# Performance work log

Measured on AMD Instinct MI355X. Metric: run time of the kernel, lower is better.

Reference implementation:

```python
import jax, jax.numpy as jnp
import numpy as np

N = 8192      # total nodes = B * NPG
D = 512       # in_dim = hidden_dim = out_dim
E = 131072    # edges
B = 16        # graphs (selected_idx batch)
NPG = 512     # nodes per graph
S = 128       # selected nodes per graph
L = 3         # conv layers
EPS = 1e-5


def setup_inputs() -> dict:
    key = jax.random.key(0)
    ks = jax.random.split(key, 16)
    scale = 0.02
    return {
        "x": jax.random.normal(ks[0], (N, D), dtype=jnp.float32),
        "edge_index": jax.random.randint(ks[1], (2, E), 0, N),
        "selected_idx": jax.random.randint(ks[2], (B, S), 0, NPG),
        "edge_label": jax.random.randint(ks[3], (E,), 0, 4),
        # per-layer EdgeConv MLP params (stacked over L layers)
        "conv_W1": jax.random.normal(ks[4], (L, 2 * D, D), dtype=jnp.float32) * scale,
        "conv_b1": jnp.full((L, D), 0.01, dtype=jnp.float32),
        "conv_W2": jax.random.normal(ks[5], (L, D, D), dtype=jnp.float32) * scale,
        "conv_b2": jnp.full((L, D), 0.01, dtype=jnp.float32),
        # shared layer norms
        "ln1_g": jnp.ones((D,), dtype=jnp.float32),
        "ln1_b": jnp.zeros((D,), dtype=jnp.float32),
        "ln2_g": jnp.ones((D,), dtype=jnp.float32),
        "ln2_b": jnp.zeros((D,), dtype=jnp.float32),
        # final FFN
        "ffn_W1": jax.random.normal(ks[6], (D, D), dtype=jnp.float32) * scale,
        "ffn_b1": jnp.full((D,), 0.01, dtype=jnp.float32),
        "ffn_W2": jax.random.normal(ks[7], (D, D), dtype=jnp.float32) * scale,
        "ffn_b2": jnp.full((D,), 0.01, dtype=jnp.float32),
    }


def _layer_norm(x, g, b):
    mu = jnp.mean(x, axis=-1, keepdims=True)
    var = jnp.mean(jnp.square(x - mu), axis=-1, keepdims=True)
    return (x - mu) * jax.lax.rsqrt(var + EPS) * g + b


def reference(x, edge_index, selected_idx, edge_label,
              conv_W1, conv_b1, conv_W2, conv_b2,
              ln1_g, ln1_b, ln2_g, ln2_b,
              ffn_W1, ffn_b1, ffn_W2, ffn_b2):
    src = edge_index[0]  # x_j source nodes
    dst = edge_index[1]  # x_i target nodes (aggregation index)
    for l in range(L):
        residual = x
        h = _layer_norm(x, ln1_g, ln1_b)
        hi = h[dst]                                   # [E, D]
        hj = h[src]                                   # [E, D]
        ef = jnp.concatenate([hi, hj - hi], axis=1)   # [E, 2D]
        m = jnp.maximum(ef @ conv_W1[l] + conv_b1[l], 0.0) @ conv_W2[l] + conv_b2[l]
        agg = jax.ops.segment_max(m, dst, num_segments=N)  # max-aggregate [N, D]
        agg = jnp.where(jnp.isfinite(agg), agg, 0.0)       # nodes w/o in-edges -> 0
        x = jnp.maximum(agg, 0.0) + residual
    residual = x
    h = _layer_norm(x, ln2_g, ln2_b)
    y = jnp.maximum(h @ ffn_W1 + ffn_b1, 0.0) @ ffn_W2 + ffn_b2
    x = y + residual
    x = x.reshape(B, NPG, D)
    idx = jnp.broadcast_to(selected_idx[:, :, None], (B, S, D))
    return jnp.take_along_axis(x, idx, axis=1)  # [B, S, D]
```

## Files before the change

### kernel.cpp

```cpp
#include <hip/hip_runtime.h>
#include <stdint.h>

#define NN 8192
#define DD 512
#define EE 131072
#define BBATCH 16
#define NPG 512
#define SSEL 128
#define LL 3

typedef unsigned short u16;
typedef __bf16 bf16x8 __attribute__((ext_vector_type(8)));
typedef float f32x4 __attribute__((ext_vector_type(4)));
typedef float f32x2 __attribute__((ext_vector_type(2)));
typedef u16 u16x8 __attribute__((ext_vector_type(8)));

__device__ __forceinline__ float bf2f(u16 u) {
    union { unsigned i; float f; } v; v.i = ((unsigned)u) << 16; return v.f;
}
__device__ __forceinline__ u16 f2bf(float f) {
    union { unsigned i; float f; } v; v.f = f;
    unsigned i = v.i;
    return (u16)((i + 0x7FFFu + ((i >> 16) & 1u)) >> 16);
}

__device__ __forceinline__ unsigned pk_bf16(float s0, float s1) {
#if __has_builtin(__builtin_amdgcn_cvt_pk_bf16_f32)
    typedef __bf16 bf16x2 __attribute__((ext_vector_type(2)));
    union { bf16x2 v; unsigned u; } r;
    r.v = __builtin_amdgcn_cvt_pk_bf16_f32(s0, s1);
    return r.u;
#else
    unsigned r0 = __float_as_uint(s0);
    r0 = (r0 + 0x7FFFu + ((r0 >> 16) & 1u)) >> 16;
    unsigned r1 = __float_as_uint(s1);
    r1 = (r1 + 0x7FFFu + ((r1 >> 16) & 1u)) & 0xffff0000u;
    return r0 | r1;
#endif
}

__device__ __forceinline__ void async_cp16(const u16* g, u16* l) {
    __builtin_amdgcn_global_load_lds(
        (const __attribute__((address_space(1))) unsigned int*)g,
        (__attribute__((address_space(3))) unsigned int*)l, 16, 0, 0);
}

__global__ __launch_bounds__(256) void ln_fused(const float* __restrict__ xin,
                                                float* __restrict__ agg_io,
                                                float* __restrict__ xout,
                                                const float* __restrict__ g,
                                                const float* __restrict__ b,
                                                u16* __restrict__ h, int doAdd) {
    int row = blockIdx.x * 4 + (threadIdx.x >> 6);
    int lane = threadIdx.x & 63;
    const f32x4* x4 = (const f32x4*)(xin + (size_t)row * DD);
    f32x4 p = x4[lane * 2], q = x4[lane * 2 + 1];
    if (doAdd) {
        const f32x4* a4 = (const f32x4*)(agg_io + (size_t)row * DD);
        f32x4 pa = a4[lane * 2], qa = a4[lane * 2 + 1];
        #pragma unroll
        for (int i = 0; i < 4; ++i) { p[i] += pa[i]; q[i] += qa[i]; }
    }
    if (agg_io) {
        f32x4 z;
        #pragma unroll
        for (int i = 0; i < 4; ++i) z[i] = 0.f;
        f32x4* a4 = (f32x4*)(agg_io + (size_t)row * DD);
        a4[lane * 2] = z;
        a4[lane * 2 + 1] = z;
    }
    f32x4* xo = (f32x4*)(xout + (size_t)row * DD);
    xo[lane * 2] = p;
    xo[lane * 2 + 1] = q;
    float v[8];
    v[0] = p[0]; v[1] = p[1]; v[2] = p[2]; v[3] = p[3];
    v[4] = q[0]; v[5] = q[1]; v[6] = q[2]; v[7] = q[3];
    float s = 0.f, sq = 0.f;
    #pragma unroll
    for (int i = 0; i < 8; ++i) { s += v[i]; sq += v[i] * v[i]; }
    #pragma unroll
    for (int o = 32; o >= 1; o >>= 1) { s += __shfl_xor(s, o); sq += __shfl_xor(sq, o); }
    float mu = s * (1.f / DD);
    float var = sq * (1.f / DD) - mu * mu;
    float rs = rsqrtf(var + 1e-5f);
    int kb = lane * 8;
    u16x8 o8;
    #pragma unroll
    for (int i = 0; i < 8; ++i) o8[i] = f2bf((v[i] - mu) * rs * g[kb + i] + b[kb + i]);
    *(u16x8*)(h + (size_t)row * DD + kb) = o8;
}

__global__ void hist_kernel(const int* __restrict__ dst, int* __restrict__ cnt) {
    int e = blockIdx.x * 256 + threadIdx.x;
    if (e < EE) atomicAdd(&cnt[dst[e]], 1);
}

__global__ __launch_bounds__(1024) void scan_kernel(const int* __restrict__ cnt,
                                                    int* __restrict__ off,
                                                    int* __restrict__ cur) {
    __shared__ int part[1024];
    int t = threadIdx.x;
    int base = t * 8;
    int loc[8]; int s = 0;
    #pragma unroll
    for (int i = 0; i < 8; ++i) { loc[i] = s; s += cnt[base + i]; }
    part[t] = s;
    __syncthreads();
    for (int o = 1; o < 1024; o <<= 1) {
        int v = part[t];
        int u = (t >= o) ? part[t - o] : 0;
        __syncthreads();
        part[t] = v + u;
        __syncthreads();
    }
    int bx = (t > 0) ? part[t - 1] : 0;
    #pragma unroll
    for (int i = 0; i < 8; ++i) { off[base + i] = bx + loc[i]; cur[base + i] = bx + loc[i]; }
    if (t == 0) off[NN] = part[1023];
}

__global__ void scatter_kernel(const int* __restrict__ src, const int* __restrict__ dst,
                               int* __restrict__ cur, int* __restrict__ ssrc,
                               int* __restrict__ sdst) {
    int e = blockIdx.x * 256 + threadIdx.x;
    if (e < EE) {
        int d = dst[e];
        int p = atomicAdd(&cur[d], 1);
        ssrc[p] = src[e];
        sdst[p] = d;
    }
}

struct CvtJobs {
    const float* s[5];
    u16* d[5];
};
__global__ __launch_bounds__(256) void cvt_t5_kernel(CvtJobs jobs) {
    __shared__ u16 tile[32][33];
    const float* src = jobs.s[blockIdx.z];
    u16* dstp = jobs.d[blockIdx.z];
    int bk = blockIdx.x * 32, bn = blockIdx.y * 32;
    int tx = threadIdx.x & 31, ty = threadIdx.x >> 5;
    #pragma unroll
    for (int r = 0; r < 32; r += 8)
        tile[ty + r][tx] = f2bf(src[(size_t)(bk + ty + r) * 512 + bn + tx]);
    __syncthreads();
    #pragma unroll
    for (int r = 0; r < 32; r += 8)
        dstp[(size_t)(bn + ty + r) * 512 + bk + tx] = tile[tx][ty + r];
}

__global__ __launch_bounds__(256) void cvt_w1_kernel(const float* __restrict__ W1g,
                                                     u16* __restrict__ dstg) {
    __shared__ u16 tile[32][33];
    const float* W1 = W1g + (size_t)blockIdx.z * 1024 * 512;
    u16* dstp = dstg + (size_t)blockIdx.z * 1024 * 512;
    int bk = blockIdx.x * 32, bn = blockIdx.y * 32;
    int tx = threadIdx.x & 31, ty = threadIdx.x >> 5;
    #pragma unroll
    for (int r = 0; r < 32; r += 8) {
        int k = bk + ty + r, n = bn + tx;
        float v = (n < 512) ? (W1[(size_t)k * 512 + n] - W1[(size_t)(k + 512) * 512 + n])
                            : W1[(size_t)(k + 512) * 512 + (n - 512)];
        tile[ty + r][tx] = f2bf(v);
    }
    __syncthreads();
    #pragma unroll
    for (int r = 0; r < 32; r += 8)
        dstp[(size_t)(bn + ty + r) * 512 + bk + tx] = tile[tx][ty + r];
}

template <int EMODE>
__global__ __launch_bounds__(256) void gemm_async(
    const u16* __restrict__ A, const u16* __restrict__ BT,
    const float* __restrict__ bias, const float* __restrict__ resid,
    void* __restrict__ Cout, int K, int ldc) {
    __shared__ u16 lA[128 * 64];
    __shared__ u16 lB[128 * 64];
    const int tid = threadIdx.x;
    const int lane = tid & 63, wave = tid >> 6;
    const int wm = wave & 1, wn = wave >> 1;
    const int quad = lane >> 4, lm = lane & 15;
    const int tileM = blockIdx.x, tileN = blockIdx.y;

    const int g = (lane & 7) ^ (lane >> 3);
    const u16* ap[4];
    const u16* bp[4];
    u16* lad[4];
    u16* lbd[4];
    #pragma unroll
    for (int j = 0; j < 4; ++j) {
        int seg = wave * 4 + j;
        int rA = tileM * 128 + seg * 8 + (lane >> 3);
        int rB = tileN * 128 + seg * 8 + (lane >> 3);
        ap[j] = A + (size_t)rA * K + g * 8;
        bp[j] = BT + (size_t)rB * K + g * 8;
        lad[j] = lA + seg * 512;
        lbd[j] = lB + seg * 512;
    }

    f32x4 acc[4][4];
    #pragma unroll
    for (int mt = 0; mt < 4; ++mt)
        #pragma unroll
        for (int nt = 0; nt < 4; ++nt)
            #pragma unroll
            for (int j = 0; j < 4; ++j) acc[mt][nt][j] = 0.f;

    for (int kb = 0; kb < K; kb += 64) {
        #pragma unroll
        for (int j = 0; j < 4; ++j) {
            async_cp16(ap[j], lad[j]);
            async_cp16(bp[j], lbd[j]);
            ap[j] += 64;
            bp[j] += 64;
        }
        __syncthreads();
        #pragma unroll
        for (int kk = 0; kk < 64; kk += 32) {
            bf16x8 af[4], bfr[4];
            int gbase = (kk >> 3) + quad;
            #pragma unroll
            for (int mt = 0; mt < 4; ++mt) {
                int row = wm * 64 + mt * 16 + lm;
                af[mt] = *(const bf16x8*)(lA + row * 64 + ((gbase ^ (row & 7)) << 3));
            }
            #pragma unroll
            for (int nt = 0; nt < 4; ++nt) {
                int row = wn * 64 + nt * 16 + lm;
                bfr[nt] = *(const bf16x8*)(lB + row * 64 + ((gbase ^ (row & 7)) << 3));
            }
            #pragma unroll
            for (int mt = 0; mt < 4; ++mt)
                #pragma unroll
                for (int nt = 0; nt < 4; ++nt)
                    acc[mt][nt] = __builtin_amdgcn_mfma_f32_16x16x32_bf16(
                        af[mt], bfr[nt], acc[mt][nt], 0, 0, 0);
        }
        __syncthreads();
    }
    #pragma unroll
    for (int mt = 0; mt < 4; ++mt) {
        #pragma unroll
        for (int nt = 0; nt < 4; ++nt) {
            int col = tileN * 128 + wn * 64 + nt * 16 + lm;
            float bv;
            if (EMODE == 2) bv = 0.f;
            else if (EMODE == 3) bv = (col < 512) ? bias[col] : 0.f;
            else bv = bias[col];
            #pragma unroll
            for (int j = 0; j < 4; ++j) {
                int grow = tileM * 128 + wm * 64 + mt * 16 + quad * 4 + j;
                float v = acc[mt][nt][j] + bv;
                if (EMODE == 0) {
                    ((u16*)Cout)[(size_t)grow * ldc + col] = f2bf(fmaxf(v, 0.f));
                } else if (EMODE == 1) {
                    ((float*)Cout)[(size_t)grow * ldc + col] =
                        v + resid[(size_t)grow * ldc + col];
                } else {
                    ((u16*)Cout)[(size_t)grow * ldc + col] = f2bf(v);
                }
            }
        }
    }
}

__global__ __launch_bounds__(512, 4) void gemm_edge(
    const u16* __restrict__ P, const int* __restrict__ ssrc,
    const int* __restrict__ sdst, const u16* __restrict__ W2T,
    const float* __restrict__ b2, float* __restrict__ agg) {
    __shared__ u16 smem[128 * 64 + 256 * 64];
    __shared__ int nid_l[128];
    u16* lA = smem;
    u16* lB = smem + 128 * 64;
    const int tid = threadIdx.x;
    const int lane = tid & 63, wave = tid >> 6;
    const int wm = wave & 1, wn = wave >> 1;
    const int quad = lane >> 4, lm = lane & 15;
    const int tileN = blockIdx.x;
    const int ebase = blockIdx.y * 128;

    if (tid < 128) nid_l[tid] = sdst[ebase + tid];

    const int g = (lane & 7) ^ (lane >> 3);
    int aoff[2], boff[2];
    u16* lout[2];
    #pragma unroll
    for (int j = 0; j < 2; ++j) {
        int seg = wave * 2 + j;
        int row = seg * 8 + (lane >> 3);
        int dn = sdst[ebase + row];
        int sn = ssrc[ebase + row];
        aoff[j] = dn * 1024 + g * 8;
        boff[j] = sn * 1024 + 512 + g * 8;
        lout[j] = lA + seg * 512 + lane * 8;
    }
    int woff[4];
    u16* lbd[4];
    #pragma unroll
    for (int j = 0; j < 4; ++j) {
        int seg = wave * 4 + j;
        int row = tileN * 256 + seg * 8 + (lane >> 3);
        woff[j] = row * 512 + g * 8;
        lbd[j] = lB + seg * 512;
    }

    f32x4 acc[4][4];
    #pragma unroll
    for (int mt = 0; mt < 4; ++mt)
        #pragma unroll
        for (int nt = 0; nt < 4; ++nt)
            #pragma unroll
            for (int j = 0; j < 4; ++j) acc[mt][nt][j] = 0.f;

    for (int kb = 0; kb < 512; kb += 64) {
        u16x8 ga[2], gb[2];
        #pragma unroll
        for (int j = 0; j < 2; ++j) {
            ga[j] = *(const u16x8*)(P + aoff[j] + kb);
            gb[j] = *(const u16x8*)(P + boff[j] + kb);
        }
        #pragma unroll
        for (int j = 0; j < 4; ++j) async_cp16(W2T + woff[j] + kb, lbd[j]);
        #pragma unroll
        for (int j = 0; j < 2; ++j) {
            union { u16x8 v; unsigned w[4]; } ua, ub;
            ua.v = ga[j];
            ub.v = gb[j];
            unsigned o[4];
            #pragma unroll
            for (int q = 0; q < 4; ++q) {
                f32x2 a, c;
                a[0] = __uint_as_float(ua.w[q] << 16);
                a[1] = __uint_as_float(ua.w[q] & 0xffff0000u);
                c[0] = __uint_as_float(ub.w[q] << 16);
                c[1] = __uint_as_float(ub.w[q] & 0xffff0000u);
                f32x2 s = a + c;
#if __has_builtin(__builtin_elementwise_max)
                f32x2 z; z[0] = 0.f; z[1] = 0.f;
                s = __builtin_elementwise_max(s, z);
#else
                s[0] = fmaxf(s[0], 0.f);
                s[1] = fmaxf(s[1], 0.f);
#endif
                o[q] = pk_bf16(s[0], s[1]);
            }
            *(uint4*)lout[j] = make_uint4(o[0], o[1], o[2], o[3]);
        }
        __syncthreads();
        #pragma unroll
        for (int kk = 0; kk < 64; kk += 32) {
            bf16x8 af[4], bfr[4];
            int gbase = (kk >> 3) + quad;
            #pragma unroll
            for (int mt = 0; mt < 4; ++mt) {
                int row = wm * 64 + mt * 16 + lm;
                af[mt] = *(const bf16x8*)(lA + row * 64 + ((gbase ^ (row & 7)) << 3));
            }
            #pragma unroll
            for (int nt = 0; nt < 4; ++nt) {
                int row = wn * 64 + nt * 16 + lm;
                bfr[nt] = *(const bf16x8*)(lB + row * 64 + ((gbase ^ (row & 7)) << 3));
            }
            #pragma unroll
            for (int mt = 0; mt < 4; ++mt)
                #pragma unroll
                for (int nt = 0; nt < 4; ++nt)
                    acc[mt][nt] = __builtin_amdgcn_mfma_f32_16x16x32_bf16(
                        af[mt], bfr[nt], acc[mt][nt], 0, 0, 0);
        }
        __syncthreads();
    }

    u16* cbuf = smem;
    for (int p = 0; p < 2; ++p) {
        if (wm == p) {
            #pragma unroll
            for (int nt = 0; nt < 4; ++nt) {
                int lcol = wn * 64 + nt * 16 + lm;
                float bv = b2[tileN * 256 + lcol];
                #pragma unroll
                for (int mt = 0; mt < 4; ++mt) {
                    #pragma unroll
                    for (int j2 = 0; j2 < 4; ++j2) {
                        int row = mt * 16 + quad * 4 + j2;
                        cbuf[row * 264 + lcol] = f2bf(fmaxf(acc[mt][nt][j2] + bv, 0.f));
                    }
                }
            }
        }
        __syncthreads();
        {
            int lcol = tid & 255;
            int gcol = tileN * 256 + lcol;
            int r0 = (tid >> 8) * 32;
            int gr0 = p * 64 + r0;
            int cur = nid_l[gr0];
            float run = bf2f(cbuf[r0 * 264 + lcol]);
            for (int r = 1; r < 32; ++r) {
                int nd = nid_l[gr0 + r];
                float v = bf2f(cbuf[(r0 + r) * 264 + lcol]);
                if (nd != cur) {
                    atomicMax((unsigned int*)&agg[(size_t)cur * DD + gcol],
                              __float_as_uint(run));
                    cur = nd;
                    run = v;
                } else {
                    run = fmaxf(run, v);
                }
            }
            atomicMax((unsigned int*)&agg[(size_t)cur * DD + gcol],
                      __float_as_uint(run));
        }
        __syncthreads();
    }
}

__global__ __launch_bounds__(128) void gather_fused(const float* __restrict__ x,
                                                    const float* __restrict__ agg,
                                                    const int* __restrict__ sel,
                                                    float* __restrict__ xs) {
    int i = blockIdx.x;
    int b = i >> 7;
    int r = b * NPG + sel[i];
    const f32x4* srcp = (const f32x4*)(x + (size_t)r * DD);
    const f32x4* aggp = (const f32x4*)(agg + (size_t)r * DD);
    f32x4 v = srcp[threadIdx.x];
    f32x4 a = aggp[threadIdx.x];
    #pragma unroll
    for (int j = 0; j < 4; ++j) v[j] += a[j];
    ((f32x4*)(xs + (size_t)i * DD))[threadIdx.x] = v;
}

extern "C" void kernel_launch(void* const* d_in, const int* in_sizes, int n_in,
                              void* d_out, int out_size, void* d_ws, size_t ws_size,
                              hipStream_t stream) {
    const float* x_in = (const float*)d_in[0];
    const int* ei = (const int*)d_in[1];
    const int* sel = (const int*)d_in[2];
    const float* W1 = (const float*)d_in[4];
    const float* b1 = (const float*)d_in[5];
    const float* W2 = (const float*)d_in[6];
    const float* b2 = (const float*)d_in[7];
    const float* g1 = (const float*)d_in[8];
    const float* be1 = (const float*)d_in[9];
    const float* g2 = (const float*)d_in[10];
    const float* be2 = (const float*)d_in[11];
    const float* fW1 = (const float*)d_in[12];
    const float* fb1 = (const float*)d_in[13];
    const float* fW2 = (const float*)d_in[14];
    const float* fb2 = (const float*)d_in[15];
    float* out = (float*)d_out;

    char* w = (char*)d_ws;
    size_t off = 0;
    auto alloc = [&](size_t bytes) -> char* {
        char* p = w + off;
        off += (bytes + 255) & ~(size_t)255;
        return p;
    };
    float* xbuf = (float*)alloc((size_t)NN * DD * 4);
    float* agg  = (float*)alloc((size_t)NN * DD * 4);
    u16* h      = (u16*)alloc((size_t)NN * DD * 2);
    u16* P      = (u16*)alloc((size_t)NN * 1024 * 2);
    u16* W1T    = (u16*)alloc((size_t)LL * 1024 * DD * 2);
    u16* W2T    = (u16*)alloc((size_t)LL * DD * DD * 2);
    u16* FW1T   = (u16*)alloc((size_t)DD * DD * 2);
    u16* FW2T   = (u16*)alloc((size_t)DD * DD * 2);
    int* cnt    = (int*)alloc((size_t)NN * 4);
    int* offs   = (int*)alloc((size_t)(NN + 1) * 4);
    int* cur    = (int*)alloc((size_t)NN * 4);
    int* ssrc   = (int*)alloc((size_t)EE * 4);
    int* sdst   = (int*)alloc((size_t)EE * 4);
    float* xs   = (float*)alloc((size_t)BBATCH * SSEL * DD * 4);
    u16* hs     = (u16*)alloc((size_t)BBATCH * SSEL * DD * 2);
    u16* uu     = (u16*)alloc((size_t)BBATCH * SSEL * DD * 2);

    const int* esrc = ei;
    const int* edst = ei + EE;

    hipMemsetAsync(cnt, 0, (size_t)NN * 4, stream);
    hist_kernel<<<EE / 256, 256, 0, stream>>>(edst, cnt);
    scan_kernel<<<1, 1024, 0, stream>>>(cnt, offs, cur);
    scatter_kernel<<<EE / 256, 256, 0, stream>>>(esrc, edst, cur, ssrc, sdst);

    cvt_w1_kernel<<<dim3(16, 32, LL), 256, 0, stream>>>(W1, W1T);
    {
        CvtJobs jobs;
        jobs.s[0] = W2;
        jobs.s[1] = W2 + (size_t)DD * DD;
        jobs.s[2] = W2 + (size_t)2 * DD * DD;
        jobs.s[3] = fW1;
        jobs.s[4] = fW2;
        jobs.d[0] = W2T;
        jobs.d[1] = W2T + (size_t)DD * DD;
        jobs.d[2] = W2T + (size_t)2 * DD * DD;
        jobs.d[3] = FW1T;
        jobs.d[4] = FW2T;
        cvt_t5_kernel<<<dim3(16, 16, 5), 256, 0, stream>>>(jobs);
    }

    for (int l = 0; l < LL; ++l) {
        ln_fused<<<NN / 4, 256, 0, stream>>>(l == 0 ? x_in : xbuf, agg, xbuf, g1, be1,
                                             h, l > 0 ? 1 : 0);
        {
            dim3 grid(NN / 128, 1024 / 128);
            gemm_async<3><<<grid, 256, 0, stream>>>(
                h, W1T + (size_t)l * 1024 * DD, b1 + (size_t)l * DD, nullptr, P, DD,
                1024);
        }
        gemm_edge<<<dim3(2, EE / 128), 512, 0, stream>>>(
            P, ssrc, sdst, W2T + (size_t)l * DD * DD, b2 + (size_t)l * DD, agg);
    }

    gather_fused<<<BBATCH * SSEL, 128, 0, stream>>>(xbuf, agg, sel, xs);
    ln_fused<<<BBATCH * SSEL / 4, 256, 0, stream>>>(xs, nullptr, xs, g2, be2, hs, 0);
    dim3 gridf(BBATCH * SSEL / 128, DD / 128);
    gemm_async<0><<<gridf, 256, 0, stream>>>(hs, FW1T, fb1, nullptr, uu, DD, DD);
    gemm_async<1><<<gridf, 256, 0, stream>>>(uu, FW2T, fb2, xs, out, DD, DD);
}
```

Before: 550.2 us.

## Double-buffer edge GEMM LDS tiles and software-pipeline gathers with MFMA

Converts the edge GEMM main loop into a double-buffered software pipeline. The W2 tile is copied asynchronously one step ahead, the node-feature gathers run two steps ahead in registers, and explicit waitcnt plus s_barrier replace the two __syncthreads per iteration. The goal is to hide gather and global-load latency behind MFMA work and to halve the barrier count. In exchange it doubles LDS use and lowers the launch-bounds occupancy hint from 4 to 2, and it relies on hand-counted vmcnt values being correct.

```diff
diff --git a/kernel.cpp b/kernel.cpp
--- a/kernel.cpp
+++ b/kernel.cpp
@@ -265,14 +265,14 @@
     }
 }
 
-__global__ __launch_bounds__(512, 4) void gemm_edge(
+__global__ __launch_bounds__(512, 2) void gemm_edge(
     const u16* __restrict__ P, const int* __restrict__ ssrc,
     const int* __restrict__ sdst, const u16* __restrict__ W2T,
     const float* __restrict__ b2, float* __restrict__ agg) {
-    __shared__ u16 smem[128 * 64 + 256 * 64];
+    __shared__ u16 smem[2 * 128 * 64 + 2 * 256 * 64];
     __shared__ int nid_l[128];
     u16* lA = smem;
-    u16* lB = smem + 128 * 64;
+    u16* lB = smem + 2 * 128 * 64;
     const int tid = threadIdx.x;
     const int lane = tid & 63, wave = tid >> 6;
     const int wm = wave & 1, wn = wave >> 1;
@@ -283,8 +283,7 @@
     if (tid < 128) nid_l[tid] = sdst[ebase + tid];
 
     const int g = (lane & 7) ^ (lane >> 3);
-    int aoff[2], boff[2];
-    u16* lout[2];
+    int aoff[2], boff[2], lout[2];
     #pragma unroll
     for (int j = 0; j < 2; ++j) {
         int seg = wave * 2 + j;
@@ -293,16 +292,15 @@
         int sn = ssrc[ebase + row];
         aoff[j] = dn * 1024 + g * 8;
         boff[j] = sn * 1024 + 512 + g * 8;
-        lout[j] = lA + seg * 512 + lane * 8;
-    }
-    int woff[4];
-    u16* lbd[4];
+        lout[j] = seg * 512 + lane * 8;
+    }
+    int woff[4], lbo[4];
     #pragma unroll
     for (int j = 0; j < 4; ++j) {
         int seg = wave * 4 + j;
         int row = tileN * 256 + seg * 8 + (lane >> 3);
         woff[j] = row * 512 + g * 8;
-        lbd[j] = lB + seg * 512;
+        lbo[j] = seg * 512;
     }
 
     f32x4 acc[4][4];
@@ -313,20 +311,26 @@
             #pragma unroll
             for (int j = 0; j < 4; ++j) acc[mt][nt][j] = 0.f;
 
-    for (int kb = 0; kb < 512; kb += 64) {
-        u16x8 ga[2], gb[2];
+    u16x8 sa[2][2], sb[2][2];
+
+    auto gather = [&](int kslot, int par) {
         #pragma unroll
         for (int j = 0; j < 2; ++j) {
-            ga[j] = *(const u16x8*)(P + aoff[j] + kb);
-            gb[j] = *(const u16x8*)(P + boff[j] + kb);
-        }
-        #pragma unroll
-        for (int j = 0; j < 4; ++j) async_cp16(W2T + woff[j] + kb, lbd[j]);
+            sa[par][j] = *(const u16x8*)(P + aoff[j] + kslot * 64);
+            sb[par][j] = *(const u16x8*)(P + boff[j] + kslot * 64);
+        }
+    };
+    auto asyncB = [&](int kslot, int par) {
+        #pragma unroll
+        for (int j = 0; j < 4; ++j)
+            async_cp16(W2T + woff[j] + kslot * 64, lB + par * 16384 + lbo[j]);
+    };
+    auto combine = [&](int par) {
         #pragma unroll
         for (int j = 0; j < 2; ++j) {
             union { u16x8 v; unsigned w[4]; } ua, ub;
-            ua.v = ga[j];
-            ub.v = gb[j];
+            ua.v = sa[par][j];
+            ub.v = sb[par][j];
             unsigned o[4];
             #pragma unroll
             for (int q = 0; q < 4; ++q) {
@@ -345,9 +349,12 @@
 #endif
                 o[q] = pk_bf16(s[0], s[1]);
             }
-            *(uint4*)lout[j] = make_uint4(o[0], o[1], o[2], o[3]);
-        }
-        __syncthreads();
+            *(uint4*)(lA + par * 8192 + lout[j]) = make_uint4(o[0], o[1], o[2], o[3]);
+        }
+    };
+    auto mfma_phase = [&](int par) {
+        const u16* la = lA + par * 8192;
+        const u16* lb = lB + par * 16384;
         #pragma unroll
         for (int kk = 0; kk < 64; kk += 32) {
             bf16x8 af[4], bfr[4];
@@ -355,12 +362,12 @@
             #pragma unroll
             for (int mt = 0; mt < 4; ++mt) {
                 int row = wm * 64 + mt * 16 + lm;
-                af[mt] = *(const bf16x8*)(lA + row * 64 + ((gbase ^ (row & 7)) << 3));
+                af[mt] = *(const bf16x8*)(la + row * 64 + ((gbase ^ (row & 7)) << 3));
             }
             #pragma unroll
             for (int nt = 0; nt < 4; ++nt) {
                 int row = wn * 64 + nt * 16 + lm;
-                bfr[nt] = *(const bf16x8*)(lB + row * 64 + ((gbase ^ (row & 7)) << 3));
+                bfr[nt] = *(const bf16x8*)(lb + row * 64 + ((gbase ^ (row & 7)) << 3));
             }
             #pragma unroll
             for (int mt = 0; mt < 4; ++mt)
@@ -369,7 +376,32 @@
                     acc[mt][nt] = __builtin_amdgcn_mfma_f32_16x16x32_bf16(
                         af[mt], bfr[nt], acc[mt][nt], 0, 0, 0);
         }
-        __syncthreads();
+    };
+
+    gather(0, 0);
+    asyncB(0, 0);
+    __builtin_amdgcn_sched_barrier(0);
+    gather(1, 1);
+    __builtin_amdgcn_sched_barrier(0);
+    combine(0);
+    asm volatile("s_waitcnt vmcnt(4) lgkmcnt(0)" ::: "memory");
+    __builtin_amdgcn_s_barrier();
+
+    #pragma unroll
+    for (int kb = 0; kb < 8; ++kb) {
+        const int cur = kb & 1, nxt = cur ^ 1;
+        if (kb < 7) asyncB(kb + 1, nxt);
+        __builtin_amdgcn_sched_barrier(0);
+        if (kb < 6) gather(kb + 2, cur);
+        __builtin_amdgcn_sched_barrier(0);
+        mfma_phase(cur);
+        if (kb < 7) combine(nxt);
+        if (kb < 6) {
+            asm volatile("s_waitcnt vmcnt(4) lgkmcnt(0)" ::: "memory");
+        } else {
+            asm volatile("s_waitcnt vmcnt(0) lgkmcnt(0)" ::: "memory");
+        }
+        __builtin_amdgcn_s_barrier();
     }
 
     u16* cbuf = smem;
```

Result: slower. 685.8 us (+24.7%).

## Pipeline gathered edge loads via async LDS staging and remap block order

Applied to the files above, without the earlier changes.

In the edge GEMM, the source-node half of P is now prefetched one K-step ahead into a per-wave LDS staging buffer with async copies. Explicit vmcnt/lgkmcnt waits and raw s_barrier calls replace __syncthreads, and setprio raises priority during the MFMA phase. The grid is flattened and remapped so that groups of 8 edge blocks run both N tiles close together, which should improve L2 reuse of the gathered rows. This adds 16KB of LDS and relies on fragile hand-placed wait counts, which could reduce occupancy or introduce races.

```diff
diff --git a/kernel.cpp b/kernel.cpp
--- a/kernel.cpp
+++ b/kernel.cpp
@@ -269,22 +269,24 @@
     const u16* __restrict__ P, const int* __restrict__ ssrc,
     const int* __restrict__ sdst, const u16* __restrict__ W2T,
     const float* __restrict__ b2, float* __restrict__ agg) {
-    __shared__ u16 smem[128 * 64 + 256 * 64];
+    __shared__ u16 smem[128 * 64 + 256 * 64 + 8192];
     __shared__ int nid_l[128];
     u16* lA = smem;
     u16* lB = smem + 128 * 64;
+    u16* stg = smem + 128 * 64 + 256 * 64;
     const int tid = threadIdx.x;
     const int lane = tid & 63, wave = tid >> 6;
     const int wm = wave & 1, wn = wave >> 1;
     const int quad = lane >> 4, lm = lane & 15;
-    const int tileN = blockIdx.x;
-    const int ebase = blockIdx.y * 128;
+    const int id = blockIdx.x;
+    const int tileN = (id >> 3) & 1;
+    const int eblk = ((id >> 4) << 3) | (id & 7);
+    const int ebase = eblk * 128;
 
     if (tid < 128) nid_l[tid] = sdst[ebase + tid];
 
     const int g = (lane & 7) ^ (lane >> 3);
-    int aoff[2], boff[2];
-    u16* lout[2];
+    int aoff[2], boff[2], lout[2];
     #pragma unroll
     for (int j = 0; j < 2; ++j) {
         int seg = wave * 2 + j;
@@ -293,17 +295,18 @@
         int sn = ssrc[ebase + row];
         aoff[j] = dn * 1024 + g * 8;
         boff[j] = sn * 1024 + 512 + g * 8;
-        lout[j] = lA + seg * 512 + lane * 8;
-    }
-    int woff[4];
-    u16* lbd[4];
+        lout[j] = seg * 512 + lane * 8;
+    }
+    int woff[4], lbo[4];
     #pragma unroll
     for (int j = 0; j < 4; ++j) {
         int seg = wave * 4 + j;
         int row = tileN * 256 + seg * 8 + (lane >> 3);
         woff[j] = row * 512 + g * 8;
-        lbd[j] = lB + seg * 512;
-    }
+        lbo[j] = seg * 512;
+    }
+    u16* stgw = stg + wave * 1024;
+    const u16* stgr = stgw + lane * 8;
 
     f32x4 acc[4][4];
     #pragma unroll
@@ -313,20 +316,28 @@
             #pragma unroll
             for (int j = 0; j < 4; ++j) acc[mt][nt][j] = 0.f;
 
-    for (int kb = 0; kb < 512; kb += 64) {
-        u16x8 ga[2], gb[2];
-        #pragma unroll
-        for (int j = 0; j < 2; ++j) {
-            ga[j] = *(const u16x8*)(P + aoff[j] + kb);
-            gb[j] = *(const u16x8*)(P + boff[j] + kb);
-        }
-        #pragma unroll
-        for (int j = 0; j < 4; ++j) async_cp16(W2T + woff[j] + kb, lbd[j]);
+    asm volatile("s_waitcnt vmcnt(0) lgkmcnt(0)" ::: "memory");
+    #pragma unroll
+    for (int j = 0; j < 2; ++j) async_cp16(P + boff[j], stgw + j * 512);
+
+    #pragma unroll
+    for (int kb = 0; kb < 8; ++kb) {
+        u16x8 ga[2];
+        #pragma unroll
+        for (int j = 0; j < 2; ++j)
+            ga[j] = *(const u16x8*)(P + aoff[j] + kb * 64);
+        __builtin_amdgcn_sched_barrier(0);
+        #pragma unroll
+        for (int j = 0; j < 4; ++j)
+            async_cp16(W2T + woff[j] + kb * 64, lB + lbo[j]);
+        __builtin_amdgcn_sched_barrier(0);
+        asm volatile("s_waitcnt vmcnt(4)" ::: "memory");
+        __builtin_amdgcn_sched_barrier(0);
         #pragma unroll
         for (int j = 0; j < 2; ++j) {
             union { u16x8 v; unsigned w[4]; } ua, ub;
             ua.v = ga[j];
-            ub.v = gb[j];
+            ub.v = *(const u16x8*)(stgr + j * 512);
             unsigned o[4];
             #pragma unroll
             for (int q = 0; q < 4; ++q) {
@@ -345,9 +356,23 @@
 #endif
                 o[q] = pk_bf16(s[0], s[1]);
             }
-            *(uint4*)lout[j] = make_uint4(o[0], o[1], o[2], o[3]);
-        }
-        __syncthreads();
+            *(uint4*)(lA + lout[j]) = make_uint4(o[0], o[1], o[2], o[3]);
+        }
+        asm volatile("s_waitcnt lgkmcnt(0)" ::: "memory");
+        __builtin_amdgcn_sched_barrier(0);
+        if (kb < 7) {
+            #pragma unroll
+            for (int j = 0; j < 2; ++j)
+                async_cp16(P + boff[j] + (kb + 1) * 64, stgw + j * 512);
+        }
+        __builtin_amdgcn_sched_barrier(0);
+        if (kb < 7) {
+            asm volatile("s_waitcnt vmcnt(4) lgkmcnt(0)" ::: "memory");
+        } else {
+            asm volatile("s_waitcnt vmcnt(0) lgkmcnt(0)" ::: "memory");
+        }
+        __builtin_amdgcn_s_barrier();
+        __builtin_amdgcn_s_setprio(1);
         #pragma unroll
         for (int kk = 0; kk < 64; kk += 32) {
             bf16x8 af[4], bfr[4];
@@ -369,7 +394,9 @@
                     acc[mt][nt] = __builtin_amdgcn_mfma_f32_16x16x32_bf16(
                         af[mt], bfr[nt], acc[mt][nt], 0, 0, 0);
         }
-        __syncthreads();
+        __builtin_amdgcn_s_setprio(0);
+        asm volatile("s_waitcnt lgkmcnt(0)" ::: "memory");
+        __builtin_amdgcn_s_barrier();
     }
 
     u16* cbuf = smem;
@@ -509,7 +536,7 @@
                 h, W1T + (size_t)l * 1024 * DD, b1 + (size_t)l * DD, nullptr, P, DD,
                 1024);
         }
-        gemm_edge<<<dim3(2, EE / 128), 512, 0, stream>>>(
+        gemm_edge<<<(EE / 128) * 2, 512, 0, stream>>>(
             P, ssrc, sdst, W2T + (size_t)l * DD * DD, b2 + (size_t)l * DD, agg);
     }
 
```

Result: slower. 594.6 us (+8.1%).

## Retile edge GEMM to 64 edges by full 512 columns per block

Applied to the files above, without the earlier changes.

Changes the edge-MLP second GEMM from 128-edge x 256-column tiles (two column blocks per edge tile) to 64-edge x 512-column tiles covering the whole output width. Each gathered/relu'd P row is now loaded and converted once instead of twice, and the segment-max reduction scans 64 rows per column with one pass instead of two half-passes, which should cut atomics. The cost is more W2 traffic per edge, since each block streams the full 512x512 weight for only 64 edges, and the launch grid gets larger.

```diff
diff --git a/kernel.cpp b/kernel.cpp
--- a/kernel.cpp
+++ b/kernel.cpp
@@ -269,40 +269,32 @@
     const u16* __restrict__ P, const int* __restrict__ ssrc,
     const int* __restrict__ sdst, const u16* __restrict__ W2T,
     const float* __restrict__ b2, float* __restrict__ agg) {
-    __shared__ u16 smem[128 * 64 + 256 * 64];
-    __shared__ int nid_l[128];
+    __shared__ u16 smem[64 * 64 + 512 * 64];
+    __shared__ int nid_l[64];
     u16* lA = smem;
-    u16* lB = smem + 128 * 64;
+    u16* lB = smem + 64 * 64;
     const int tid = threadIdx.x;
     const int lane = tid & 63, wave = tid >> 6;
-    const int wm = wave & 1, wn = wave >> 1;
     const int quad = lane >> 4, lm = lane & 15;
-    const int tileN = blockIdx.x;
-    const int ebase = blockIdx.y * 128;
-
-    if (tid < 128) nid_l[tid] = sdst[ebase + tid];
+    const int ebase = blockIdx.x * 64;
+
+    if (tid < 64) nid_l[tid] = sdst[ebase + tid];
 
     const int g = (lane & 7) ^ (lane >> 3);
-    int aoff[2], boff[2];
-    u16* lout[2];
-    #pragma unroll
-    for (int j = 0; j < 2; ++j) {
-        int seg = wave * 2 + j;
-        int row = seg * 8 + (lane >> 3);
+    int aoff, boff, lout;
+    {
+        int row = wave * 8 + (lane >> 3);
         int dn = sdst[ebase + row];
         int sn = ssrc[ebase + row];
-        aoff[j] = dn * 1024 + g * 8;
-        boff[j] = sn * 1024 + 512 + g * 8;
-        lout[j] = lA + seg * 512 + lane * 8;
-    }
-    int woff[4];
-    u16* lbd[4];
-    #pragma unroll
-    for (int j = 0; j < 4; ++j) {
-        int seg = wave * 4 + j;
-        int row = tileN * 256 + seg * 8 + (lane >> 3);
-        woff[j] = row * 512 + g * 8;
-        lbd[j] = lB + seg * 512;
+        aoff = dn * 1024 + g * 8;
+        boff = sn * 1024 + 512 + g * 8;
+        lout = wave * 512 + lane * 8;
+    }
+    int wbase, lbbase;
+    {
+        int row0 = wave * 64 + (lane >> 3);
+        wbase = row0 * 512 + g * 8;
+        lbbase = wave * 4096;
     }
 
     f32x4 acc[4][4];
@@ -314,19 +306,15 @@
             for (int j = 0; j < 4; ++j) acc[mt][nt][j] = 0.f;
 
     for (int kb = 0; kb < 512; kb += 64) {
-        u16x8 ga[2], gb[2];
-        #pragma unroll
-        for (int j = 0; j < 2; ++j) {
-            ga[j] = *(const u16x8*)(P + aoff[j] + kb);
-            gb[j] = *(const u16x8*)(P + boff[j] + kb);
-        }
-        #pragma unroll
-        for (int j = 0; j < 4; ++j) async_cp16(W2T + woff[j] + kb, lbd[j]);
-        #pragma unroll
-        for (int j = 0; j < 2; ++j) {
+        u16x8 ga = *(const u16x8*)(P + aoff + kb);
+        u16x8 gb = *(const u16x8*)(P + boff + kb);
+        #pragma unroll
+        for (int j = 0; j < 8; ++j)
+            async_cp16(W2T + wbase + j * 4096 + kb, lB + lbbase + j * 512);
+        {
             union { u16x8 v; unsigned w[4]; } ua, ub;
-            ua.v = ga[j];
-            ub.v = gb[j];
+            ua.v = ga;
+            ub.v = gb;
             unsigned o[4];
             #pragma unroll
             for (int q = 0; q < 4; ++q) {
@@ -345,7 +333,7 @@
 #endif
                 o[q] = pk_bf16(s[0], s[1]);
             }
-            *(uint4*)lout[j] = make_uint4(o[0], o[1], o[2], o[3]);
+            *(uint4*)(lA + lout) = make_uint4(o[0], o[1], o[2], o[3]);
         }
         __syncthreads();
         #pragma unroll
@@ -354,12 +342,12 @@
             int gbase = (kk >> 3) + quad;
             #pragma unroll
             for (int mt = 0; mt < 4; ++mt) {
-                int row = wm * 64 + mt * 16 + lm;
+                int row = mt * 16 + lm;
                 af[mt] = *(const bf16x8*)(lA + row * 64 + ((gbase ^ (row & 7)) << 3));
             }
             #pragma unroll
             for (int nt = 0; nt < 4; ++nt) {
-                int row = wn * 64 + nt * 16 + lm;
+                int row = wave * 64 + nt * 16 + lm;
                 bfr[nt] = *(const bf16x8*)(lB + row * 64 + ((gbase ^ (row & 7)) << 3));
             }
             #pragma unroll
@@ -373,46 +361,38 @@
     }
 
     u16* cbuf = smem;
-    for (int p = 0; p < 2; ++p) {
-        if (wm == p) {
-            #pragma unroll
-            for (int nt = 0; nt < 4; ++nt) {
-                int lcol = wn * 64 + nt * 16 + lm;
-                float bv = b2[tileN * 256 + lcol];
-                #pragma unroll
-                for (int mt = 0; mt < 4; ++mt) {
-                    #pragma unroll
-                    for (int j2 = 0; j2 < 4; ++j2) {
-                        int row = mt * 16 + quad * 4 + j2;
-                        cbuf[row * 264 + lcol] = f2bf(fmaxf(acc[mt][nt][j2] + bv, 0.f));
-                    }
-                }
-            }
-        }
-        __syncthreads();
-        {
-            int lcol = tid & 255;
-            int gcol = tileN * 256 + lcol;
-            int r0 = (tid >> 8) * 32;
-            int gr0 = p * 64 + r0;
-            int cur = nid_l[gr0];
-            float run = bf2f(cbuf[r0 * 264 + lcol]);
-            for (int r = 1; r < 32; ++r) {
-                int nd = nid_l[gr0 + r];
-                float v = bf2f(cbuf[(r0 + r) * 264 + lcol]);
-                if (nd != cur) {
-                    atomicMax((unsigned int*)&agg[(size_t)cur * DD + gcol],
-                              __float_as_uint(run));
-                    cur = nd;
-                    run = v;
-                } else {
-                    run = fmaxf(run, v);
-                }
-            }
-            atomicMax((unsigned int*)&agg[(size_t)cur * DD + gcol],
-                      __float_as_uint(run));
-        }
-        __syncthreads();
+    #pragma unroll
+    for (int nt = 0; nt < 4; ++nt) {
+        int col = wave * 64 + nt * 16 + lm;
+        float bv = b2[col];
+        #pragma unroll
+        for (int mt = 0; mt < 4; ++mt) {
+            #pragma unroll
+            for (int j2 = 0; j2 < 4; ++j2) {
+                int row = mt * 16 + quad * 4 + j2;
+                cbuf[row * 520 + col] = f2bf(fmaxf(acc[mt][nt][j2] + bv, 0.f));
+            }
+        }
+    }
+    __syncthreads();
+    {
+        int col = tid;
+        int cur = nid_l[0];
+        float run = bf2f(cbuf[col]);
+        for (int r = 1; r < 64; ++r) {
+            int nd = nid_l[r];
+            float v = bf2f(cbuf[r * 520 + col]);
+            if (nd != cur) {
+                atomicMax((unsigned int*)&agg[(size_t)cur * DD + col],
+                          __float_as_uint(run));
+                cur = nd;
+                run = v;
+            } else {
+                run = fmaxf(run, v);
+            }
+        }
+        atomicMax((unsigned int*)&agg[(size_t)cur * DD + col],
+                  __float_as_uint(run));
     }
 }
 
@@ -509,7 +489,7 @@
                 h, W1T + (size_t)l * 1024 * DD, b1 + (size_t)l * DD, nullptr, P, DD,
                 1024);
         }
-        gemm_edge<<<dim3(2, EE / 128), 512, 0, stream>>>(
+        gemm_edge<<<EE / 64, 512, 0, stream>>>(
             P, ssrc, sdst, W2T + (size_t)l * DD * DD, b2 + (size_t)l * DD, agg);
     }
 
```

Measured after the change: 551.0 us. Within noise of the previous version (+0.1%).
